# Kernel tuning notes

Hardware: AMD Instinct MI355X
Metric: run time of the kernel (lower is better)

## Reference

```python
import jax, jax.numpy as jnp
import numpy as np

N = 100000   # num_nodes
E = 3200000  # num_edges
F = 7        # node_features
H = 128      # hidden_dim
D = 64       # embedding_dim
EPS = 1e-5


def setup_inputs() -> dict:
    key = jax.random.key(0)
    ks = jax.random.split(key, 32)
    inp = {}
    inp["x"] = jax.random.normal(ks[0], (N, F), jnp.float32)
    inp["edge_index"] = jax.random.randint(ks[1], (2, E), 0, N, dtype=jnp.int64)
    # input projection
    inp["W_in"] = jax.random.normal(ks[2], (F, H), jnp.float32) * 0.1
    inp["b_in"] = jax.random.normal(ks[3], (H,), jnp.float32) * 0.01
    # 3 GCN layers: 128->128, 128->128, 128->64, each with eval-mode BatchNorm params
    dims = [(H, H), (H, H), (H, D)]
    for i, (di, do) in enumerate(dims):
        k = jax.random.split(ks[4 + i], 6)
        inp[f"W{i}"] = jax.random.normal(k[0], (di, do), jnp.float32) * (1.0 / np.sqrt(di))
        inp[f"b{i}"] = jax.random.normal(k[1], (do,), jnp.float32) * 0.01
        inp[f"g{i}"] = 1.0 + 0.1 * jax.random.normal(k[2], (do,), jnp.float32)
        inp[f"be{i}"] = 0.1 * jax.random.normal(k[3], (do,), jnp.float32)
        inp[f"m{i}"] = 0.1 * jax.random.normal(k[4], (do,), jnp.float32)
        inp[f"v{i}"] = jax.random.uniform(k[5], (do,), jnp.float32, 0.5, 1.5)
    return inp


def _gcn_conv(x, W, b, src, dst, dinv):
    h = x @ W                                   # [N, do]
    coef = dinv[src] * dinv[dst]                # [E]
    agg = jax.ops.segment_sum(h[src] * coef[:, None], dst, num_segments=N)
    # self-loop contribution: norm = dinv[i]^2
    return agg + h * (dinv * dinv)[:, None] + b


def _bn_eval(x, g, be, m, v):
    return (x - m) * (g * jax.lax.rsqrt(v + EPS)) + be


def reference(x, edge_index, W_in, b_in,
              W0, b0, g0, be0, m0, v0,
              W1, b1, g1, be1, m1, v1,
              W2, b2, g2, be2, m2, v2):
    src, dst = edge_index[0], edge_index[1]
    # in-degree with self-loops (same for all layers)
    deg = jax.ops.segment_sum(jnp.ones((E,), x.dtype), dst, num_segments=N) + 1.0
    dinv = jax.lax.rsqrt(deg)

    h = jax.nn.relu(x @ W_in + b_in)            # [N, H]

    # layer 0: conv -> bn -> relu -> (dropout=id, eval) -> residual
    h0 = _gcn_conv(h, W0, b0, src, dst, dinv)
    h0 = jax.nn.relu(_bn_eval(h0, g0, be0, m0, v0)) + h
    # layer 1
    h1 = _gcn_conv(h0, W1, b1, src, dst, dinv)
    h1 = jax.nn.relu(_bn_eval(h1, g1, be1, m1, v1)) + h0
    # layer 2 (final): conv -> bn only (shape changes to D, no residual/relu)
    h2 = _gcn_conv(h1, W2, b2, src, dst, dinv)
    return _bn_eval(h2, g2, be2, m2, v2)        # [N, D]
```

## Files before the change

kernel.cpp:

```cpp
#include <hip/hip_runtime.h>


#define NN 100000
#define NE 3200000
#define FI 7
#define HD 128
#define DD 64
#define EPS 1e-5f
#define NB 196
#define EPB 8192
#define NBLK ((NE + EPB - 1) / EPB)

typedef float float2v __attribute__((ext_vector_type(2)));
typedef short short8 __attribute__((ext_vector_type(8)));
typedef float f32x4 __attribute__((ext_vector_type(4)));

__device__ __forceinline__ unsigned char f2fp8(float f) {
    return (unsigned char)(__builtin_amdgcn_cvt_pk_fp8_f32(f, f, 0, false) & 0xFF);
}
__device__ __forceinline__ unsigned short f2bf(float f) {
    unsigned u = __float_as_uint(f);
    u += 0x7FFF + ((u >> 16) & 1);
    return (unsigned short)(u >> 16);
}


__global__ __launch_bounds__(256) void p1_bucket_hist(const int* __restrict__ ei,
                                                      int* __restrict__ bcnt,
                                                      int* __restrict__ blk_off) {
    __shared__ int h[NB];
    const int t = threadIdx.x;
    for (int b = t; b < NB; b += 256) h[b] = 0;
    __syncthreads();
    const int base = blockIdx.x * EPB;
#pragma unroll 4
    for (int i = 0; i < EPB / 256; ++i) {
        int e = base + i * 256 + t;
        if (e < NE) atomicAdd(&h[ei[NE + e] >> 9], 1);
    }
    __syncthreads();
    for (int b = t; b < NB; b += 256) {
        int c = h[b];
        blk_off[blockIdx.x * NB + b] = c ? atomicAdd(&bcnt[b], c) : 0;
    }
}

__global__ __launch_bounds__(256) void p2_bucket_scan(const int* __restrict__ bcnt,
                                                      int* __restrict__ bstart) {
    __shared__ int sh[256];
    const int t = threadIdx.x;
    const int myc = (t < NB) ? bcnt[t] : 0;
    sh[t] = myc;
    __syncthreads();
    for (int off = 1; off < 256; off <<= 1) {
        int v = (t >= off) ? sh[t - off] : 0;
        __syncthreads();
        sh[t] += v;
        __syncthreads();
    }
    if (t < NB) bstart[t] = sh[t] - myc;
    if (t == 0) bstart[NB] = NE;
}

__global__ __launch_bounds__(256) void p3_bin(const int* __restrict__ ei,
                                              const int* __restrict__ bstart,
                                              const int* __restrict__ blk_off,
                                              int* __restrict__ ebin) {
    __shared__ int cur[NB];
    const int t = threadIdx.x;
    for (int b = t; b < NB; b += 256)
        cur[b] = bstart[b] + blk_off[blockIdx.x * NB + b];
    __syncthreads();
    const int base = blockIdx.x * EPB;
#pragma unroll 4
    for (int i = 0; i < EPB / 256; ++i) {
        int e = base + i * 256 + t;
        if (e < NE) {
            int s = ei[e];
            int d = ei[NE + e];
            int p = atomicAdd(&cur[d >> 9], 1);
            ebin[p] = ((d & 511) << 23) | s;
        }
    }
}

__global__ __launch_bounds__(512) void p4_finalize(const int* __restrict__ bstart,
                                                   const int* __restrict__ ebin,
                                                   int* __restrict__ esrc,
                                                   int* __restrict__ rowstart,
                                                   float* __restrict__ dinv) {
    __shared__ int lh[512];
    __shared__ int sc[512];
    __shared__ int lc[512];
    const int t = threadIdx.x;
    const int b = blockIdx.x;
    const int n0 = b << 9;
    const int ebase = bstart[b];
    const int ecnt = bstart[b + 1] - ebase;
    lh[t] = 0;
    __syncthreads();
    for (int i = t; i < ecnt; i += 512)
        atomicAdd(&lh[((unsigned)ebin[ebase + i]) >> 23], 1);
    __syncthreads();
    const int c = lh[t];
    sc[t] = c;
    __syncthreads();
    for (int off = 1; off < 512; off <<= 1) {
        int v = (t >= off) ? sc[t - off] : 0;
        __syncthreads();
        sc[t] += v;
        __syncthreads();
    }
    const int excl = ebase + sc[t] - c;
    lc[t] = excl;
    const int node = n0 + t;
    if (node < NN) {
        rowstart[node] = excl;
        dinv[node] = rsqrtf((float)c + 1.0f);
    }
    if (b == NB - 1 && t == 0) rowstart[NN] = NE;
    __syncthreads();
    for (int i = t; i < ecnt; i += 512) {
        int v = ebin[ebase + i];
        int p = atomicAdd(&lc[((unsigned)v) >> 23], 1);
        esrc[p] = v & 0x7FFFFF;
    }
}


__global__ __launch_bounds__(256) void inproj_kernel(const float* __restrict__ x,
                                                     const float* __restrict__ W_in,
                                                     const float* __restrict__ b_in,
                                                     float* __restrict__ hA,
                                                     unsigned short* __restrict__ hAbf) {
    int n = blockIdx.x * 2 + (threadIdx.x >> 7);
    int j = threadIdx.x & 127;
    float acc = b_in[j];
#pragma unroll
    for (int f = 0; f < FI; ++f) acc += x[n * FI + f] * W_in[f * HD + j];
    acc = fmaxf(acc, 0.f);
    hA[n * HD + j] = acc;
    hAbf[n * HD + j] = f2bf(acc);
}


template <int DO>
__global__ __launch_bounds__(64) void wprep(const float* __restrict__ W,
                                            unsigned short* __restrict__ Wf) {
    const int lane = threadIdx.x;
    const int nt = blockIdx.x >> 2;
    const int ks = blockIdx.x & 3;
    short8 o;
#pragma unroll
    for (int j = 0; j < 8; ++j)
        o[j] = (short)f2bf(W[(ks * 32 + (lane >> 4) * 8 + j) * DO + nt * 16 + (lane & 15)]);
    *(short8*)(Wf + ((size_t)blockIdx.x * 64 + lane) * 8) = o;
}


template <int DO>
__global__ __launch_bounds__(256) void gemm_mfma(const unsigned short* __restrict__ A,
                                                 const unsigned short* __restrict__ Wf,
                                                 unsigned char* __restrict__ B) {
    constexpr int CT = DO / 64;
    const int tid = threadIdx.x;
    const int wave = tid >> 6;
    const int lane = tid & 63;
    const int n0 = blockIdx.x * 32;
    short8 bfrag[CT][4];
#pragma unroll
    for (int ct = 0; ct < CT; ++ct)
#pragma unroll
        for (int ks = 0; ks < 4; ++ks)
            bfrag[ct][ks] = *(const short8*)(Wf + ((size_t)(((wave * CT + ct) * 4 + ks) * 64) + lane) * 8);
#pragma unroll
    for (int rt = 0; rt < 2; ++rt) {
        const int arow = n0 + rt * 16 + (lane & 15);
        short8 afrag[4];
#pragma unroll
        for (int ks = 0; ks < 4; ++ks)
            afrag[ks] = *(const short8*)(A + (size_t)arow * HD + ks * 32 + ((lane >> 4) & 3) * 8);
        f32x4 acc[CT];
#pragma unroll
        for (int ct = 0; ct < CT; ++ct) acc[ct] = (f32x4){0.f, 0.f, 0.f, 0.f};
#pragma unroll
        for (int ks = 0; ks < 4; ++ks)
#pragma unroll
            for (int ct = 0; ct < CT; ++ct)
                acc[ct] = __builtin_amdgcn_mfma_f32_16x16x32_bf16(afrag[ks], bfrag[ct][ks], acc[ct], 0, 0, 0);
#pragma unroll
        for (int ct = 0; ct < CT; ++ct) {
            const int ocol = (wave * CT + ct) * 16 + (lane & 15);
#pragma unroll
            for (int r = 0; r < 4; ++r) {
                const int orow = n0 + rt * 16 + (lane >> 4) * 4 + r;
                B[(size_t)orow * DO + ocol] = f2fp8(acc[ct][r]);
            }
        }
    }
}


template <int DO, bool RELU_RES>
__global__ __launch_bounds__(128) void gather_kernel(const unsigned char* __restrict__ hXW,
                                                     float* __restrict__ resOut,
                                                     unsigned short* __restrict__ resBf,
                                                     const int* __restrict__ rowstart,
                                                     const int* __restrict__ esrc,
                                                     const float* __restrict__ dinv,
                                                     const float* __restrict__ bias,
                                                     const float* __restrict__ g,
                                                     const float* __restrict__ be,
                                                     const float* __restrict__ m,
                                                     const float* __restrict__ v) {
    constexpr int CG = DO / 8;
    constexpr int NG = 128 / CG;
    constexpr int QN = DO / 4;
    __shared__ int s_idx[128];
    __shared__ float s_dv[128];
    __shared__ float4 s_red[128][2];
    const int n = blockIdx.x;
    const int t = threadIdx.x;
    const int rs = rowstart[n];
    const int re = rowstart[n + 1];
    const float dn = dinv[n];
    const int q = t & (CG - 1);
    const int grp = t / CG;
    float4 a0l = {0.f, 0.f, 0.f, 0.f}, a0h = {0.f, 0.f, 0.f, 0.f};
    float4 a1l = {0.f, 0.f, 0.f, 0.f}, a1h = {0.f, 0.f, 0.f, 0.f};
    for (int base = rs; base < re; base += 128) {
        const int c = min(128, re - base);
        __syncthreads();
        if (t < c) {
            int s = esrc[base + t];
            s_idx[t] = s;
            s_dv[t] = dinv[s];
        }
        __syncthreads();
        for (int j = grp; j < c; j += 2 * NG) {
            {
                const uint2 u = *(const uint2*)(hXW + (size_t)s_idx[j] * DO + q * 8);
                const float w = s_dv[j];
                const float2v l0 = __builtin_amdgcn_cvt_pk_f32_fp8(u.x, false);
                const float2v h0 = __builtin_amdgcn_cvt_pk_f32_fp8(u.x, true);
                const float2v l1 = __builtin_amdgcn_cvt_pk_f32_fp8(u.y, false);
                const float2v h1 = __builtin_amdgcn_cvt_pk_f32_fp8(u.y, true);
                a0l.x += l0.x * w; a0l.y += l0.y * w; a0l.z += h0.x * w; a0l.w += h0.y * w;
                a0h.x += l1.x * w; a0h.y += l1.y * w; a0h.z += h1.x * w; a0h.w += h1.y * w;
            }
            if (j + NG < c) {
                const uint2 u = *(const uint2*)(hXW + (size_t)s_idx[j + NG] * DO + q * 8);
                const float w = s_dv[j + NG];
                const float2v l0 = __builtin_amdgcn_cvt_pk_f32_fp8(u.x, false);
                const float2v h0 = __builtin_amdgcn_cvt_pk_f32_fp8(u.x, true);
                const float2v l1 = __builtin_amdgcn_cvt_pk_f32_fp8(u.y, false);
                const float2v h1 = __builtin_amdgcn_cvt_pk_f32_fp8(u.y, true);
                a1l.x += l0.x * w; a1l.y += l0.y * w; a1l.z += h0.x * w; a1l.w += h0.y * w;
                a1h.x += l1.x * w; a1h.y += l1.y * w; a1h.z += h1.x * w; a1h.w += h1.y * w;
            }
        }
    }
    a0l.x += a1l.x; a0l.y += a1l.y; a0l.z += a1l.z; a0l.w += a1l.w;
    a0h.x += a1h.x; a0h.y += a1h.y; a0h.z += a1h.z; a0h.w += a1h.w;
    s_red[t][0] = a0l;
    s_red[t][1] = a0h;
    __syncthreads();
    if (t < QN) {
        const int qq = t >> 1, h = t & 1;
        float4 sum = s_red[qq][h];
#pragma unroll
        for (int k = 1; k < NG; ++k) {
            const float4 a = s_red[k * CG + qq][h];
            sum.x += a.x; sum.y += a.y; sum.z += a.z; sum.w += a.w;
        }
        const unsigned su = *(const unsigned*)(hXW + (size_t)n * DO + t * 4);
        const float2v slo = __builtin_amdgcn_cvt_pk_f32_fp8(su, false);
        const float2v shi = __builtin_amdgcn_cvt_pk_f32_fp8(su, true);
        const float4 b4 = *(const float4*)(bias + t * 4);
        const float4 g4 = *(const float4*)(g + t * 4);
        const float4 be4 = *(const float4*)(be + t * 4);
        const float4 m4 = *(const float4*)(m + t * 4);
        const float4 v4 = *(const float4*)(v + t * 4);
        float4 val;
        val.x = (sum.x + dn * slo.x) * dn + b4.x;
        val.y = (sum.y + dn * slo.y) * dn + b4.y;
        val.z = (sum.z + dn * shi.x) * dn + b4.z;
        val.w = (sum.w + dn * shi.y) * dn + b4.w;
        val.x = (val.x - m4.x) * (g4.x * rsqrtf(v4.x + EPS)) + be4.x;
        val.y = (val.y - m4.y) * (g4.y * rsqrtf(v4.y + EPS)) + be4.y;
        val.z = (val.z - m4.z) * (g4.z * rsqrtf(v4.z + EPS)) + be4.z;
        val.w = (val.w - m4.w) * (g4.w * rsqrtf(v4.w + EPS)) + be4.w;
        float4* outp = (float4*)(resOut + (size_t)n * DO + t * 4);
        if (RELU_RES) {
            const float4 r = *outp;
            val.x = fmaxf(val.x, 0.f) + r.x;
            val.y = fmaxf(val.y, 0.f) + r.y;
            val.z = fmaxf(val.z, 0.f) + r.z;
            val.w = fmaxf(val.w, 0.f) + r.w;
            ushort4 bf;
            bf.x = f2bf(val.x); bf.y = f2bf(val.y);
            bf.z = f2bf(val.z); bf.w = f2bf(val.w);
            *(ushort4*)(resBf + (size_t)n * DO + t * 4) = bf;
        }
        *outp = val;
    }
}


extern "C" void kernel_launch(void* const* d_in, const int* in_sizes, int n_in,
                              void* d_out, int out_size, void* d_ws, size_t ws_size,
                              hipStream_t stream) {
    const float* x    = (const float*)d_in[0];
    const int*   ei   = (const int*)d_in[1];
    const float* W_in = (const float*)d_in[2];
    const float* b_in = (const float*)d_in[3];
    const float* Wl[3] = {(const float*)d_in[4], (const float*)d_in[10], (const float*)d_in[16]};
    const float* bl[3] = {(const float*)d_in[5], (const float*)d_in[11], (const float*)d_in[17]};
    const float* gl[3] = {(const float*)d_in[6], (const float*)d_in[12], (const float*)d_in[18]};
    const float* bel[3] = {(const float*)d_in[7], (const float*)d_in[13], (const float*)d_in[19]};
    const float* ml[3] = {(const float*)d_in[8], (const float*)d_in[14], (const float*)d_in[20]};
    const float* vl[3] = {(const float*)d_in[9], (const float*)d_in[15], (const float*)d_in[21]};
    float* out = (float*)d_out;

    char* ws = (char*)d_ws;
    size_t off = 0;
    auto carve = [&](size_t bytes) {
        void* p = ws + off;
        off += (bytes + 255) & ~(size_t)255;
        return p;
    };
    int*   bcnt     = (int*)carve(NB * sizeof(int));
    int*   bstart   = (int*)carve((NB + 1) * sizeof(int));
    int*   blk_off  = (int*)carve((size_t)NBLK * NB * sizeof(int));
    int*   rowstart = (int*)carve((NN + 1) * sizeof(int));
    float* dinv     = (float*)carve(NN * sizeof(float));
    int*   esrc     = (int*)carve((size_t)NE * sizeof(int));
    float* hA       = (float*)carve((size_t)NN * HD * sizeof(float));
    unsigned short* hAbf = (unsigned short*)carve((size_t)NN * HD * sizeof(unsigned short));
    unsigned char* hB = (unsigned char*)carve((size_t)NN * HD);
    int*   ebin     = (int*)carve((size_t)NE * sizeof(int));
    unsigned short* wf0 = (unsigned short*)carve((size_t)HD * HD * sizeof(unsigned short));
    unsigned short* wf1 = (unsigned short*)carve((size_t)HD * HD * sizeof(unsigned short));
    unsigned short* wf2 = (unsigned short*)carve((size_t)HD * DD * sizeof(unsigned short));
    (void)ws_size;

    hipMemsetAsync(bcnt, 0, NB * sizeof(int), stream);

    wprep<128><<<32, 64, 0, stream>>>(Wl[0], wf0);
    wprep<128><<<32, 64, 0, stream>>>(Wl[1], wf1);
    wprep<64><<<16, 64, 0, stream>>>(Wl[2], wf2);

    p1_bucket_hist<<<NBLK, 256, 0, stream>>>(ei, bcnt, blk_off);
    p2_bucket_scan<<<1, 256, 0, stream>>>(bcnt, bstart);
    p3_bin<<<NBLK, 256, 0, stream>>>(ei, bstart, blk_off, ebin);
    p4_finalize<<<NB, 512, 0, stream>>>(bstart, ebin, esrc, rowstart, dinv);

    inproj_kernel<<<NN / 2, 256, 0, stream>>>(x, W_in, b_in, hA, hAbf);

    gemm_mfma<128><<<NN / 32, 256, 0, stream>>>(hAbf, wf0, hB);
    gather_kernel<128, true><<<NN, 128, 0, stream>>>(hB, hA, hAbf, rowstart, esrc, dinv,
                                                     bl[0], gl[0], bel[0], ml[0], vl[0]);
    gemm_mfma<128><<<NN / 32, 256, 0, stream>>>(hAbf, wf1, hB);
    gather_kernel<128, true><<<NN, 128, 0, stream>>>(hB, hA, hAbf, rowstart, esrc, dinv,
                                                     bl[1], gl[1], bel[1], ml[1], vl[1]);
    gemm_mfma<64><<<NN / 32, 256, 0, stream>>>(hAbf, wf2, hB);
    gather_kernel<64, false><<<NN, 128, 0, stream>>>(hB, out, (unsigned short*)nullptr,
                                                     rowstart, esrc, dinv,
                                                     bl[2], gl[2], bel[2], ml[2], vl[2]);
}
```

Measured before the change: 534.7 us.

## Replace block-per-node gather with wave-per-node gather using shuffles

The gather/aggregation kernel now gives each node one 64-lane wavefront instead of a 128-thread block, with four nodes per 256-thread block. Neighbour indices and weights are broadcast with wave shuffles rather than staged in shared memory. The final reduction uses xor-shuffles instead of an LDS tree, which removes all __syncthreads. The aim is to cut barrier and LDS overhead and raise occupancy for the average degree of about 32. The trade-off is that each lane loads 4 bytes instead of 8 per neighbour, and high-degree nodes get less parallelism.

```diff
diff --git a/kernel.cpp b/kernel.cpp
--- a/kernel.cpp
+++ b/kernel.cpp
@@ -202,95 +202,88 @@
 
 
 template <int DO, bool RELU_RES>
-__global__ __launch_bounds__(128) void gather_kernel(const unsigned char* __restrict__ hXW,
-                                                     float* __restrict__ resOut,
-                                                     unsigned short* __restrict__ resBf,
-                                                     const int* __restrict__ rowstart,
-                                                     const int* __restrict__ esrc,
-                                                     const float* __restrict__ dinv,
-                                                     const float* __restrict__ bias,
-                                                     const float* __restrict__ g,
-                                                     const float* __restrict__ be,
-                                                     const float* __restrict__ m,
-                                                     const float* __restrict__ v) {
-    constexpr int CG = DO / 8;
-    constexpr int NG = 128 / CG;
-    constexpr int QN = DO / 4;
-    __shared__ int s_idx[128];
-    __shared__ float s_dv[128];
-    __shared__ float4 s_red[128][2];
-    const int n = blockIdx.x;
-    const int t = threadIdx.x;
+__global__ __launch_bounds__(256) void gather_wave(const unsigned char* __restrict__ hXW,
+                                                   float* __restrict__ resOut,
+                                                   unsigned short* __restrict__ resBf,
+                                                   const int* __restrict__ rowstart,
+                                                   const int* __restrict__ esrc,
+                                                   const float* __restrict__ dinv,
+                                                   const float* __restrict__ bias,
+                                                   const float* __restrict__ g,
+                                                   const float* __restrict__ be,
+                                                   const float* __restrict__ m,
+                                                   const float* __restrict__ v) {
+    constexpr int UW = DO / 4;
+    constexpr int EP = 64 / UW;
+    const int t = threadIdx.x;
+    const int lane = t & 63;
+    const int n = blockIdx.x * 4 + (t >> 6);
+    const int sub = lane / UW;
+    const int cw = lane % UW;
     const int rs = rowstart[n];
     const int re = rowstart[n + 1];
     const float dn = dinv[n];
-    const int q = t & (CG - 1);
-    const int grp = t / CG;
-    float4 a0l = {0.f, 0.f, 0.f, 0.f}, a0h = {0.f, 0.f, 0.f, 0.f};
-    float4 a1l = {0.f, 0.f, 0.f, 0.f}, a1h = {0.f, 0.f, 0.f, 0.f};
-    for (int base = rs; base < re; base += 128) {
-        const int c = min(128, re - base);
-        __syncthreads();
-        if (t < c) {
-            int s = esrc[base + t];
-            s_idx[t] = s;
-            s_dv[t] = dinv[s];
-        }
-        __syncthreads();
-        for (int j = grp; j < c; j += 2 * NG) {
-            {
-                const uint2 u = *(const uint2*)(hXW + (size_t)s_idx[j] * DO + q * 8);
-                const float w = s_dv[j];
-                const float2v l0 = __builtin_amdgcn_cvt_pk_f32_fp8(u.x, false);
-                const float2v h0 = __builtin_amdgcn_cvt_pk_f32_fp8(u.x, true);
-                const float2v l1 = __builtin_amdgcn_cvt_pk_f32_fp8(u.y, false);
-                const float2v h1 = __builtin_amdgcn_cvt_pk_f32_fp8(u.y, true);
-                a0l.x += l0.x * w; a0l.y += l0.y * w; a0l.z += h0.x * w; a0l.w += h0.y * w;
-                a0h.x += l1.x * w; a0h.y += l1.y * w; a0h.z += h1.x * w; a0h.w += h1.y * w;
+    float4 acc0 = {0.f, 0.f, 0.f, 0.f};
+    float4 acc1 = {0.f, 0.f, 0.f, 0.f};
+    for (int base = rs; base < re; base += 64) {
+        const int c = min(64, re - base);
+        int e = 0;
+        float dv = 0.f;
+        if (lane < c) {
+            e = esrc[base + lane];
+            dv = dinv[e];
+        }
+        for (int k = 0; k < c; k += 2 * EP) {
+            const int j0 = k + sub;
+            const int j1 = k + EP + sub;
+            const int s0 = __shfl(e, j0, 64);
+            const float w0 = __shfl(dv, j0, 64);
+            const int s1 = __shfl(e, j1, 64);
+            const float w1 = __shfl(dv, j1, 64);
+            if (j0 < c) {
+                const unsigned u = *(const unsigned*)(hXW + (size_t)s0 * DO + cw * 4);
+                const float2v lo = __builtin_amdgcn_cvt_pk_f32_fp8(u, false);
+                const float2v hi = __builtin_amdgcn_cvt_pk_f32_fp8(u, true);
+                acc0.x += lo.x * w0; acc0.y += lo.y * w0;
+                acc0.z += hi.x * w0; acc0.w += hi.y * w0;
             }
-            if (j + NG < c) {
-                const uint2 u = *(const uint2*)(hXW + (size_t)s_idx[j + NG] * DO + q * 8);
-                const float w = s_dv[j + NG];
-                const float2v l0 = __builtin_amdgcn_cvt_pk_f32_fp8(u.x, false);
-                const float2v h0 = __builtin_amdgcn_cvt_pk_f32_fp8(u.x, true);
-                const float2v l1 = __builtin_amdgcn_cvt_pk_f32_fp8(u.y, false);
-                const float2v h1 = __builtin_amdgcn_cvt_pk_f32_fp8(u.y, true);
-                a1l.x += l0.x * w; a1l.y += l0.y * w; a1l.z += h0.x * w; a1l.w += h0.y * w;
-                a1h.x += l1.x * w; a1h.y += l1.y * w; a1h.z += h1.x * w; a1h.w += h1.y * w;
+            if (j1 < c) {
+                const unsigned u = *(const unsigned*)(hXW + (size_t)s1 * DO + cw * 4);
+                const float2v lo = __builtin_amdgcn_cvt_pk_f32_fp8(u, false);
+                const float2v hi = __builtin_amdgcn_cvt_pk_f32_fp8(u, true);
+                acc1.x += lo.x * w1; acc1.y += lo.y * w1;
+                acc1.z += hi.x * w1; acc1.w += hi.y * w1;
             }
         }
     }
-    a0l.x += a1l.x; a0l.y += a1l.y; a0l.z += a1l.z; a0l.w += a1l.w;
-    a0h.x += a1h.x; a0h.y += a1h.y; a0h.z += a1h.z; a0h.w += a1h.w;
-    s_red[t][0] = a0l;
-    s_red[t][1] = a0h;
-    __syncthreads();
-    if (t < QN) {
-        const int qq = t >> 1, h = t & 1;
-        float4 sum = s_red[qq][h];
-#pragma unroll
-        for (int k = 1; k < NG; ++k) {
-            const float4 a = s_red[k * CG + qq][h];
-            sum.x += a.x; sum.y += a.y; sum.z += a.z; sum.w += a.w;
-        }
-        const unsigned su = *(const unsigned*)(hXW + (size_t)n * DO + t * 4);
+    acc0.x += acc1.x; acc0.y += acc1.y; acc0.z += acc1.z; acc0.w += acc1.w;
+#pragma unroll
+    for (int off = 32; off >= UW; off >>= 1) {
+        acc0.x += __shfl_xor(acc0.x, off, 64);
+        acc0.y += __shfl_xor(acc0.y, off, 64);
+        acc0.z += __shfl_xor(acc0.z, off, 64);
+        acc0.w += __shfl_xor(acc0.w, off, 64);
+    }
+    if (lane < UW) {
+        const int q = cw;
+        const unsigned su = *(const unsigned*)(hXW + (size_t)n * DO + q * 4);
         const float2v slo = __builtin_amdgcn_cvt_pk_f32_fp8(su, false);
         const float2v shi = __builtin_amdgcn_cvt_pk_f32_fp8(su, true);
-        const float4 b4 = *(const float4*)(bias + t * 4);
-        const float4 g4 = *(const float4*)(g + t * 4);
-        const float4 be4 = *(const float4*)(be + t * 4);
-        const float4 m4 = *(const float4*)(m + t * 4);
-        const float4 v4 = *(const float4*)(v + t * 4);
+        const float4 b4 = *(const float4*)(bias + q * 4);
+        const float4 g4 = *(const float4*)(g + q * 4);
+        const float4 be4 = *(const float4*)(be + q * 4);
+        const float4 m4 = *(const float4*)(m + q * 4);
+        const float4 v4 = *(const float4*)(v + q * 4);
         float4 val;
-        val.x = (sum.x + dn * slo.x) * dn + b4.x;
-        val.y = (sum.y + dn * slo.y) * dn + b4.y;
-        val.z = (sum.z + dn * shi.x) * dn + b4.z;
-        val.w = (sum.w + dn * shi.y) * dn + b4.w;
+        val.x = (acc0.x + dn * slo.x) * dn + b4.x;
+        val.y = (acc0.y + dn * slo.y) * dn + b4.y;
+        val.z = (acc0.z + dn * shi.x) * dn + b4.z;
+        val.w = (acc0.w + dn * shi.y) * dn + b4.w;
         val.x = (val.x - m4.x) * (g4.x * rsqrtf(v4.x + EPS)) + be4.x;
         val.y = (val.y - m4.y) * (g4.y * rsqrtf(v4.y + EPS)) + be4.y;
         val.z = (val.z - m4.z) * (g4.z * rsqrtf(v4.z + EPS)) + be4.z;
         val.w = (val.w - m4.w) * (g4.w * rsqrtf(v4.w + EPS)) + be4.w;
-        float4* outp = (float4*)(resOut + (size_t)n * DO + t * 4);
+        float4* outp = (float4*)(resOut + (size_t)n * DO + q * 4);
         if (RELU_RES) {
             const float4 r = *outp;
             val.x = fmaxf(val.x, 0.f) + r.x;
@@ -300,7 +293,7 @@
             ushort4 bf;
             bf.x = f2bf(val.x); bf.y = f2bf(val.y);
             bf.z = f2bf(val.z); bf.w = f2bf(val.w);
-            *(ushort4*)(resBf + (size_t)n * DO + t * 4) = bf;
+            *(ushort4*)(resBf + (size_t)n * DO + q * 4) = bf;
         }
         *outp = val;
     }
@@ -358,13 +351,13 @@
     inproj_kernel<<<NN / 2, 256, 0, stream>>>(x, W_in, b_in, hA, hAbf);
 
     gemm_mfma<128><<<NN / 32, 256, 0, stream>>>(hAbf, wf0, hB);
-    gather_kernel<128, true><<<NN, 128, 0, stream>>>(hB, hA, hAbf, rowstart, esrc, dinv,
-                                                     bl[0], gl[0], bel[0], ml[0], vl[0]);
+    gather_wave<128, true><<<NN / 4, 256, 0, stream>>>(hB, hA, hAbf, rowstart, esrc, dinv,
+                                                       bl[0], gl[0], bel[0], ml[0], vl[0]);
     gemm_mfma<128><<<NN / 32, 256, 0, stream>>>(hAbf, wf1, hB);
-    gather_kernel<128, true><<<NN, 128, 0, stream>>>(hB, hA, hAbf, rowstart, esrc, dinv,
-                                                     bl[1], gl[1], bel[1], ml[1], vl[1]);
+    gather_wave<128, true><<<NN / 4, 256, 0, stream>>>(hB, hA, hAbf, rowstart, esrc, dinv,
+                                                       bl[1], gl[1], bel[1], ml[1], vl[1]);
     gemm_mfma<64><<<NN / 32, 256, 0, stream>>>(hAbf, wf2, hB);
-    gather_kernel<64, false><<<NN, 128, 0, stream>>>(hB, out, (unsigned short*)nullptr,
-                                                     rowstart, esrc, dinv,
-                                                     bl[2], gl[2], bel[2], ml[2], vl[2]);
-}
+    gather_wave<64, false><<<NN / 4, 256, 0, stream>>>(hB, out, (unsigned short*)nullptr,
+                                                       rowstart, esrc, dinv,
+                                                       bl[2], gl[2], bel[2], ml[2], vl[2]);
+}
```

New measurement: 608.3 us. 13.8% more time.
